# Kernel optimization log

Hardware: AMD Instinct MI355X
Metric: run time of the kernel (lower is better)

Reference implementation:

```python
import jax, jax.numpy as jnp
import numpy as np

N_SRC = 100000
N_DST = 100000
N_EDGES = 300000
FEAT = 256
REV_DIM = 128
REV_VOCAB = 500000


def setup_inputs() -> dict:
    key = jax.random.key(0)
    ks = jax.random.split(key, 14)
    feat = jax.random.normal(ks[0], (N_SRC, FEAT), dtype=jnp.float32)
    cj = jax.random.uniform(ks[1], (N_SRC, 1), dtype=jnp.float32)
    ci = jax.random.uniform(ks[2], (N_DST, 1), dtype=jnp.float32)
    edge_src = jax.random.randint(ks[3], (N_EDGES,), 0, N_SRC)
    edge_dst = jax.random.randint(ks[4], (N_EDGES,), 0, N_DST)
    review_id = jax.random.randint(ks[5], (N_EDGES,), 0, REV_VOCAB)
    s = 0.05
    review_emb = jax.random.normal(ks[6], (REV_VOCAB, REV_DIM), dtype=jnp.float32) * s
    prob_w = jax.random.normal(ks[7], (1, REV_DIM), dtype=jnp.float32) * s      # prob_score
    score_w = jax.random.normal(ks[8], (1, REV_DIM), dtype=jnp.float32) * s     # review_score
    rw1 = jax.random.normal(ks[9], (FEAT, REV_DIM), dtype=jnp.float32) * s      # review_w[0]
    rw2 = jax.random.normal(ks[10], (FEAT, FEAT), dtype=jnp.float32) * s        # review_w[2]
    rw3 = jax.random.normal(ks[11], (FEAT, FEAT), dtype=jnp.float32) * s        # review_w[4]
    lin_w = jax.random.normal(ks[12], (FEAT, FEAT), dtype=jnp.float32) * s      # self.linear
    lin_b = jax.random.normal(ks[13], (FEAT,), dtype=jnp.float32) * s
    return dict(feat=feat, cj=cj, ci=ci, edge_src=edge_src, edge_dst=edge_dst,
                review_id=review_id, review_emb=review_emb, prob_w=prob_w,
                score_w=score_w, rw1=rw1, rw2=rw2, rw3=rw3, lin_w=lin_w, lin_b=lin_b)


def reference(feat, cj, ci, edge_src, edge_dst, review_id,
              review_emb, prob_w, score_w, rw1, rw2, rw3, lin_w, lin_b):
    gelu = lambda x: jax.nn.gelu(x, approximate=False)  # torch default GELU (erf)
    # gather review embeddings per edge: [E, 128]
    rfeat = review_emb[review_id]
    pa = jax.nn.sigmoid(rfeat @ prob_w.T)    # [E, 1]
    ra = jax.nn.sigmoid(rfeat @ score_w.T)   # [E, 1]
    # review_w MLP: 128 -> F -> F -> F, no bias, GELU between
    rf = gelu(gelu(rfeat @ rw1.T) @ rw2.T) @ rw3.T  # [E, F]
    # per-edge message, gated and normalized by src cj (dropout is identity at p=0)
    m = (feat[edge_src] * pa + rf * ra) * cj[edge_src]  # [E, F]
    # scatter-sum to destination nodes
    h = jax.ops.segment_sum(m, edge_dst, num_segments=N_DST)  # [N_dst, F]
    rst = h * ci
    return rst @ lin_w.T + lin_b
```

## Files before the change

kernel.cpp:

```cpp
#include <hip/hip_runtime.h>
#include <math.h>
#include <stdint.h>


typedef short bf16x8 __attribute__((ext_vector_type(8)));
typedef float f32x16 __attribute__((ext_vector_type(16)));

__device__ __forceinline__ float bf2f(unsigned short v) {
    union { unsigned int u; float f; } x; x.u = ((unsigned int)v) << 16; return x.f;
}
__device__ __forceinline__ unsigned short f2bf(float f) {
    union { float f; unsigned int u; } x; x.f = f;
    unsigned int u = x.u;
    return (unsigned short)((u + 0x7FFFu + ((u >> 16) & 1u)) >> 16);
}
__device__ __forceinline__ unsigned pack2(float lo, float hi) {
    unsigned r;
    asm("v_cvt_pk_bf16_f32 %0, %1, %2" : "=v"(r) : "v"(lo), "v"(hi));
    return r;
}
__device__ __forceinline__ float gelu_fast(float x) {
    float y = x * (0.7978845608f + 0.0356774081f * x * x);
    float e = __builtin_amdgcn_exp2f(y * 2.8853900818f);
    float th = 1.0f - 2.0f * __builtin_amdgcn_rcpf(e + 1.0f);
    return 0.5f * x * (1.0f + th);
}
__device__ __forceinline__ float sigmoidf(float x) {
    return 1.0f / (1.0f + expf(-x));
}

__global__ __launch_bounds__(256) void prep_weights(
    const float* __restrict__ rw1, const float* __restrict__ rw2,
    const float* __restrict__ rw3, const float* __restrict__ lw,
    unsigned short* __restrict__ w1s, unsigned short* __restrict__ w2s,
    unsigned short* __restrict__ w3s, unsigned short* __restrict__ lws)
{
    int i = blockIdx.x * blockDim.x + threadIdx.x;
    int j   = i & 7;
    int l   = (i >> 3) & 31;
    int kgg = (i >> 8) & 1;
    int n2  = (i >> 9) & 7;
    int ks  = i >> 12;
    if (i < 32768) {
        w1s[i] = f2bf(rw1[(n2 * 32 + l) * 128 + ks * 16 + kgg * 8 + j]);
    }
    if (i < 65536) {
        int row = n2 * 32 + l, k = ks * 16 + kgg * 8 + j;
        w2s[i] = f2bf(rw2[(size_t)row * 256 + k]);
        w3s[i] = f2bf(rw3[(size_t)row * 256 + k]);
        int ok = (k & 192) | ((k & 1) << 5) | ((k & 63) >> 1);
        lws[i] = f2bf(lw[(size_t)row * 256 + ok]);
    }
}

__device__ __forceinline__ bf16x8 ldw(const unsigned short* __restrict__ W,
                                      int ks, int nglob, int kg, int l31) {
    return *(const bf16x8*)(W + (((((ks * 8 + nglob) * 2) + kg) * 32 + l31) << 3));
}

__global__ __launch_bounds__(256) void hist_kernel(
    const int* __restrict__ edst, int* __restrict__ cnt,
    int* __restrict__ within, int E)
{
    int e = blockIdx.x * blockDim.x + threadIdx.x;
    if (e < E) within[e] = atomicAdd(&cnt[edst[e]], 1);
}

__global__ __launch_bounds__(1024) void scan_block(
    const int* __restrict__ cnt, int* __restrict__ start,
    int* __restrict__ bsum, int n)
{
    __shared__ int s[1024];
    int gid = blockIdx.x * 1024 + threadIdx.x;
    int v = (gid < n) ? cnt[gid] : 0;
    s[threadIdx.x] = v;
    __syncthreads();
    #pragma unroll
    for (int off = 1; off < 1024; off <<= 1) {
        int t = (threadIdx.x >= off) ? s[threadIdx.x - off] : 0;
        __syncthreads();
        if (threadIdx.x >= off) s[threadIdx.x] += t;
        __syncthreads();
    }
    if (gid < n) start[gid] = s[threadIdx.x] - v;
    if (threadIdx.x == 1023) bsum[blockIdx.x] = s[1023];
}

__global__ void scan_bsum(int* __restrict__ bsum, int nb) {
    if (threadIdx.x == 0 && blockIdx.x == 0) {
        int acc = 0;
        for (int i = 0; i < nb; ++i) { int v = bsum[i]; bsum[i] = acc; acc += v; }
    }
}

__global__ __launch_bounds__(1024) void add_offsets(
    int* __restrict__ start, const int* __restrict__ bsum, int n, int E)
{
    int gid = blockIdx.x * 1024 + threadIdx.x;
    if (gid < n) start[gid] += bsum[gid >> 10];
    if (gid == 0) start[n] = E;
}

__global__ __launch_bounds__(256) void build_sorted(
    const int* __restrict__ edst, const int* __restrict__ within,
    const int* __restrict__ start, const int* __restrict__ rid,
    const int* __restrict__ esrc, int* __restrict__ rid_s,
    int* __restrict__ esrc_s, int E)
{
    int e = blockIdx.x * blockDim.x + threadIdx.x;
    if (e < E) {
        int pos = start[edst[e]] + within[e];
        rid_s[pos]  = rid[e];
        esrc_s[pos] = esrc[e];
    }
}

__device__ __forceinline__ bf16x8 ldtf(const unsigned short* t_lds, int row, int ks, int kg) {
    int slot = (ks * 2 + kg) ^ (row & 15);
    return *(const bf16x8*)((const char*)t_lds + row * 512 + slot * 16);
}
__device__ __forceinline__ void sttf(unsigned short* t_lds, int row, int nn, int p, int kg, uint2 w) {
    int slot = (nn * 4 + p) ^ (row & 15);
    *(uint2*)((char*)t_lds + row * 512 + slot * 16 + kg * 8) = w;
}
__device__ __forceinline__ bf16x8 ldrb(const unsigned short* t_rb, int row, int ks, int kg) {
    int slot = (ks * 2 + kg) ^ (row & 15);
    return *(const bf16x8*)((const char*)t_rb + row * 256 + slot * 16);
}

__global__ __launch_bounds__(256, 3) void fused_edge(
    const float* __restrict__ remb, const int* __restrict__ rid_s,
    const int* __restrict__ esrc_s,
    const unsigned short* __restrict__ w1s, const unsigned short* __restrict__ w2s,
    const unsigned short* __restrict__ w3s,
    const float* __restrict__ pw, const float* __restrict__ sw,
    const float* __restrict__ cj, float* __restrict__ ga,
    unsigned short* __restrict__ m, int E)
{
    __shared__ __align__(16) unsigned short t_lds[64 * 256];
    __shared__ __align__(16) unsigned short t_rb[64 * 128];
    __shared__ float gvb_lds[64];

    const int lane = threadIdx.x & 63;
    const int f    = threadIdx.x >> 6;
    const int l31  = lane & 31;
    const int kg   = lane >> 5;
    const int blk0 = blockIdx.x * 64;

    {
        const int t = threadIdx.x;
        #pragma unroll
        for (int p = 0; p < 4; ++p) {
            int sIdx = p * 256 + t;
            int row  = sIdx >> 4;
            int c16  = sIdx & 15;
            int gr   = blk0 + row;
            int rr   = rid_s[(gr < E) ? gr : (E - 1)];
            const float* sp = remb + (size_t)rr * 128 + c16 * 8;
            float4 a = *(const float4*)sp;
            float4 b = *(const float4*)(sp + 4);
            uint4 w;
            w.x = pack2(a.x, a.y); w.y = pack2(a.z, a.w);
            w.z = pack2(b.x, b.y); w.w = pack2(b.z, b.w);
            int slot = c16 ^ (row & 15);
            *(uint4*)((char*)t_rb + row * 256 + slot * 16) = w;
        }
    }
    __syncthreads();

    {
        f32x16 acc[2][2];
        #pragma unroll
        for (int g = 0; g < 2; ++g) { acc[g][0] = (f32x16)0.0f; acc[g][1] = (f32x16)0.0f; }
        float pd0 = 0.f, rd0 = 0.f, pd1 = 0.f, rd1 = 0.f;

        #pragma unroll
        for (int ks = 0; ks < 8; ++ks) {
            bf16x8 wf0 = ldw(w1s, ks, f * 2 + 0, kg, l31);
            bf16x8 wf1 = ldw(w1s, ks, f * 2 + 1, kg, l31);
            #pragma unroll
            for (int g = 0; g < 2; ++g) {
                bf16x8 af = ldrb(t_rb, g * 32 + l31, ks, kg);
                if (f == 0) {
                    const int kk = ks * 16 + kg * 8;
                    float4 p0 = *(const float4*)(pw + kk), p1 = *(const float4*)(pw + kk + 4);
                    float4 s0 = *(const float4*)(sw + kk), s1v = *(const float4*)(sw + kk + 4);
                    float v0 = bf2f((unsigned short)af[0]), v1 = bf2f((unsigned short)af[1]);
                    float v2 = bf2f((unsigned short)af[2]), v3 = bf2f((unsigned short)af[3]);
                    float v4 = bf2f((unsigned short)af[4]), v5 = bf2f((unsigned short)af[5]);
                    float v6 = bf2f((unsigned short)af[6]), v7 = bf2f((unsigned short)af[7]);
                    float dp = v0*p0.x + v1*p0.y + v2*p0.z + v3*p0.w
                             + v4*p1.x + v5*p1.y + v6*p1.z + v7*p1.w;
                    float dr = v0*s0.x + v1*s0.y + v2*s0.z + v3*s0.w
                             + v4*s1v.x + v5*s1v.y + v6*s1v.z + v7*s1v.w;
                    if (g == 0) { pd0 += dp; rd0 += dr; } else { pd1 += dp; rd1 += dr; }
                }
                acc[g][0] = __builtin_amdgcn_mfma_f32_32x32x16_bf16(wf0, af, acc[g][0], 0, 0, 0);
                acc[g][1] = __builtin_amdgcn_mfma_f32_32x32x16_bf16(wf1, af, acc[g][1], 0, 0, 0);
            }
        }

        if (f == 0) {
            pd0 += __shfl_xor(pd0, 32); rd0 += __shfl_xor(rd0, 32);
            pd1 += __shfl_xor(pd1, 32); rd1 += __shfl_xor(rd1, 32);
            if (lane < 32) {
                int i0 = blk0 + l31, i1 = blk0 + 32 + l31;
                float cj0 = cj[esrc_s[(i0 < E) ? i0 : (E - 1)]];
                float cj1 = cj[esrc_s[(i1 < E) ? i1 : (E - 1)]];
                if (i0 < E) ga[i0] = sigmoidf(pd0) * cj0;
                if (i1 < E) ga[i1] = sigmoidf(pd1) * cj1;
                gvb_lds[l31]      = sigmoidf(rd0) * cj0;
                gvb_lds[32 + l31] = sigmoidf(rd1) * cj1;
            }
        }

        #pragma unroll
        for (int g = 0; g < 2; ++g)
            #pragma unroll
            for (int n = 0; n < 2; ++n)
                #pragma unroll
                for (int p = 0; p < 4; ++p) {
                    uint2 w;
                    w.x = pack2(gelu_fast(acc[g][n][4*p + 0]), gelu_fast(acc[g][n][4*p + 1]));
                    w.y = pack2(gelu_fast(acc[g][n][4*p + 2]), gelu_fast(acc[g][n][4*p + 3]));
                    sttf(t_lds, g * 32 + l31, f * 2 + n, p, kg, w);
                }
    }
    __syncthreads();

    {
        f32x16 acc[2][2];
        #pragma unroll
        for (int g = 0; g < 2; ++g) { acc[g][0] = (f32x16)0.0f; acc[g][1] = (f32x16)0.0f; }

        #pragma unroll
        for (int ks = 0; ks < 16; ++ks) {
            bf16x8 wf0 = ldw(w2s, ks, f * 2 + 0, kg, l31);
            bf16x8 wf1 = ldw(w2s, ks, f * 2 + 1, kg, l31);
            #pragma unroll
            for (int g = 0; g < 2; ++g) {
                bf16x8 tf = ldtf(t_lds, g * 32 + l31, ks, kg);
                acc[g][0] = __builtin_amdgcn_mfma_f32_32x32x16_bf16(wf0, tf, acc[g][0], 0, 0, 0);
                acc[g][1] = __builtin_amdgcn_mfma_f32_32x32x16_bf16(wf1, tf, acc[g][1], 0, 0, 0);
            }
        }
        __syncthreads();
        #pragma unroll
        for (int g = 0; g < 2; ++g)
            #pragma unroll
            for (int n = 0; n < 2; ++n)
                #pragma unroll
                for (int p = 0; p < 4; ++p) {
                    uint2 w;
                    w.x = pack2(gelu_fast(acc[g][n][4*p + 0]), gelu_fast(acc[g][n][4*p + 1]));
                    w.y = pack2(gelu_fast(acc[g][n][4*p + 2]), gelu_fast(acc[g][n][4*p + 3]));
                    sttf(t_lds, g * 32 + l31, f * 2 + n, p, kg, w);
                }
    }
    __syncthreads();

    {
        f32x16 acc[2][2];
        #pragma unroll
        for (int g = 0; g < 2; ++g) { acc[g][0] = (f32x16)0.0f; acc[g][1] = (f32x16)0.0f; }

        #pragma unroll
        for (int ks = 0; ks < 16; ++ks) {
            bf16x8 wf0 = ldw(w3s, ks, f * 2 + 0, kg, l31);
            bf16x8 wf1 = ldw(w3s, ks, f * 2 + 1, kg, l31);
            #pragma unroll
            for (int g = 0; g < 2; ++g) {
                bf16x8 tf = ldtf(t_lds, g * 32 + l31, ks, kg);
                acc[g][0] = __builtin_amdgcn_mfma_f32_32x32x16_bf16(tf, wf0, acc[g][0], 0, 0, 0);
                acc[g][1] = __builtin_amdgcn_mfma_f32_32x32x16_bf16(tf, wf1, acc[g][1], 0, 0, 0);
            }
        }

        #pragma unroll
        for (int g = 0; g < 2; ++g)
            #pragma unroll
            for (int r = 0; r < 16; ++r) {
                const int lrow = (r & 3) + 8 * (r >> 2) + 4 * kg;
                const int gi = blk0 + g * 32 + lrow;
                if (gi < E) {
                    float gbv = gvb_lds[g * 32 + lrow];
                    float v0 = acc[g][0][r] * gbv;
                    float v1 = acc[g][1][r] * gbv;
                    *(unsigned*)(m + (size_t)gi * 256 + f * 64 + l31 * 2) = pack2(v0, v1);
                }
            }
    }
}

__global__ __launch_bounds__(256) void segsum_kernel(
    const int* __restrict__ start, const unsigned short* __restrict__ m,
    const float* __restrict__ ga, const int* __restrict__ esrc_s,
    const float* __restrict__ feat, unsigned short* __restrict__ h, int ND)
{
    int d = blockIdx.x * 4 + (threadIdx.x >> 6);
    if (d >= ND) return;
    int lane = threadIdx.x & 63;
    int q = lane >> 4;
    int b = lane & 15;
    int foff = q * 64 + 2 * b;
    int s0 = start[d], s1 = start[d + 1];
    float a0 = 0.f, a1 = 0.f, a2 = 0.f, a3 = 0.f;
    for (int base = s0; base < s1; base += 4) {
        float gav[4], msk[4];
        const float* fp[4];
        const unsigned short* mp[4];
        #pragma unroll
        for (int j = 0; j < 4; ++j) {
            int idx = base + j;
            bool v  = idx < s1;
            int ic  = v ? idx : (s1 - 1);
            msk[j]  = v ? 1.f : 0.f;
            gav[j]  = ga[ic] * msk[j];
            fp[j]   = feat + (size_t)esrc_s[ic] * 256 + foff;
            mp[j]   = m + (size_t)ic * 256 + lane * 4;
        }
        #pragma unroll
        for (int j = 0; j < 4; ++j) {
            float2 fa = *(const float2*)fp[j];
            float2 fb = *(const float2*)(fp[j] + 32);
            ushort4 v4 = *(const ushort4*)mp[j];
            a0 += bf2f(v4.x) * msk[j] + fa.x * gav[j];
            a1 += bf2f(v4.y) * msk[j] + fb.x * gav[j];
            a2 += bf2f(v4.z) * msk[j] + fa.y * gav[j];
            a3 += bf2f(v4.w) * msk[j] + fb.y * gav[j];
        }
    }
    ushort4 o; o.x = f2bf(a0); o.y = f2bf(a1); o.z = f2bf(a2); o.w = f2bf(a3);
    *(ushort4*)(h + (size_t)d * 256 + lane * 4) = o;
}

__global__ __launch_bounds__(256, 2) void g4_kernel(
    const unsigned short* __restrict__ Ab, const unsigned short* __restrict__ lws,
    float* __restrict__ outf, const float* __restrict__ ci,
    const float* __restrict__ bias, int M)
{
    const int lane = threadIdx.x & 63;
    const int wid  = threadIdx.x >> 6;
    const int l31  = lane & 31;
    const int kg   = lane >> 5;
    const int f    = wid & 1;
    const int wbase = blockIdx.x * 128 + (wid >> 1) * 64;
    const int r0 = wbase + l31, r1 = wbase + 32 + l31;
    const int ar0 = (r0 < M) ? r0 : (M - 1);
    const int ar1 = (r1 < M) ? r1 : (M - 1);

    f32x16 acc[2][4];
    #pragma unroll
    for (int mi = 0; mi < 2; ++mi)
        #pragma unroll
        for (int n = 0; n < 4; ++n) acc[mi][n] = (f32x16)0.0f;

    #pragma unroll
    for (int ks = 0; ks < 16; ++ks) {
        const int kk = ks * 16 + kg * 8;
        bf16x8 a0 = *(const bf16x8*)(Ab + (size_t)ar0 * 256 + kk);
        bf16x8 a1 = *(const bf16x8*)(Ab + (size_t)ar1 * 256 + kk);
        #pragma unroll
        for (int n = 0; n < 4; ++n) {
            bf16x8 b = ldw(lws, ks, f * 4 + n, kg, l31);
            acc[0][n] = __builtin_amdgcn_mfma_f32_32x32x16_bf16(a0, b, acc[0][n], 0, 0, 0);
            acc[1][n] = __builtin_amdgcn_mfma_f32_32x32x16_bf16(a1, b, acc[1][n], 0, 0, 0);
        }
    }
    #pragma unroll
    for (int mi = 0; mi < 2; ++mi) {
        #pragma unroll
        for (int r = 0; r < 16; ++r) {
            const int gr = wbase + mi * 32 + (r & 3) + 8 * (r >> 2) + 4 * kg;
            if (gr >= M) continue;
            float civ = ci[gr];
            #pragma unroll
            for (int n = 0; n < 4; ++n) {
                int col = f * 128 + n * 32 + l31;
                outf[(size_t)gr * 256 + col] = acc[mi][n][r] * civ + bias[col];
            }
        }
    }
}

extern "C" void kernel_launch(void* const* d_in, const int* in_sizes, int n_in,
                              void* d_out, int out_size, void* d_ws, size_t ws_size,
                              hipStream_t stream) {
    const float* feat = (const float*)d_in[0];
    const float* cj   = (const float*)d_in[1];
    const float* ci   = (const float*)d_in[2];
    const int*   esrc = (const int*)d_in[3];
    const int*   edst = (const int*)d_in[4];
    const int*   rid  = (const int*)d_in[5];
    const float* remb = (const float*)d_in[6];
    const float* pw   = (const float*)d_in[7];
    const float* sw   = (const float*)d_in[8];
    const float* rw1  = (const float*)d_in[9];
    const float* rw2  = (const float*)d_in[10];
    const float* rw3  = (const float*)d_in[11];
    const float* lw   = (const float*)d_in[12];
    const float* lb   = (const float*)d_in[13];
    float* out = (float*)d_out;

    const int E  = in_sizes[3];
    const int ND = in_sizes[2];

    char* ws = (char*)d_ws;
    float* ga = (float*)ws;
    unsigned short* m   = (unsigned short*)(ga + E);
    unsigned short* h   = m + (size_t)E * 256;
    unsigned short* w1s = h + (size_t)ND * 256;
    unsigned short* w2s = w1s + 32768;
    unsigned short* w3s = w2s + 65536;
    unsigned short* lws = w3s + 65536;
    int* cnt    = (int*)(lws + 65536);
    int* start  = cnt + ND;
    int* bsum   = start + ND + 1;
    int* within = bsum + 128;
    int* rid_s  = within + E;
    int* esrc_s = rid_s + E;

    const int NB = (ND + 1023) / 1024;

    hipMemsetAsync(cnt, 0, (size_t)ND * sizeof(int), stream);
    prep_weights<<<256, 256, 0, stream>>>(rw1, rw2, rw3, lw, w1s, w2s, w3s, lws);

    hist_kernel<<<(E + 255) / 256, 256, 0, stream>>>(edst, cnt, within, E);
    scan_block<<<NB, 1024, 0, stream>>>(cnt, start, bsum, ND);
    scan_bsum<<<1, 64, 0, stream>>>(bsum, NB);
    add_offsets<<<NB, 1024, 0, stream>>>(start, bsum, ND, E);
    build_sorted<<<(E + 255) / 256, 256, 0, stream>>>(edst, within, start, rid, esrc,
                                                      rid_s, esrc_s, E);

    fused_edge<<<(E + 63) / 64, 256, 0, stream>>>(
        remb, rid_s, esrc_s, w1s, w2s, w3s, pw, sw, cj, ga, m, E);

    segsum_kernel<<<(ND + 3) / 4, 256, 0, stream>>>(start, m, ga, esrc_s, feat, h, ND);

    g4_kernel<<<(ND + 127) / 128, 256, 0, stream>>>(h, lws, out, ci, lb, ND);
}
```

Measured before the change: 362.3 us.

## Store edge messages in natural column order and simplify GELU to sigmoid form

The MLP epilogue now uses lane shuffles so each even lane writes two adjacent columns, which puts the message buffer in natural column order. The segment-sum kernel can then read feat with one contiguous float4 per lane instead of two strided float2 loads, and the linear weight prep no longer needs its column permutation. GELU is replaced by the cheaper x*sigmoid(1.702x) approximation, which cuts instructions but is less accurate than the tanh form. The store pattern changes to half the lanes writing 4-byte words, which may hurt store coalescing.

```diff
diff --git a/kernel.cpp b/kernel.cpp
--- a/kernel.cpp
+++ b/kernel.cpp
@@ -20,10 +20,8 @@
     return r;
 }
 __device__ __forceinline__ float gelu_fast(float x) {
-    float y = x * (0.7978845608f + 0.0356774081f * x * x);
-    float e = __builtin_amdgcn_exp2f(y * 2.8853900818f);
-    float th = 1.0f - 2.0f * __builtin_amdgcn_rcpf(e + 1.0f);
-    return 0.5f * x * (1.0f + th);
+    float e = __builtin_amdgcn_exp2f(x * -2.4554912f);
+    return x * __builtin_amdgcn_rcpf(e + 1.0f);
 }
 __device__ __forceinline__ float sigmoidf(float x) {
     return 1.0f / (1.0f + expf(-x));
@@ -48,8 +46,7 @@
         int row = n2 * 32 + l, k = ks * 16 + kgg * 8 + j;
         w2s[i] = f2bf(rw2[(size_t)row * 256 + k]);
         w3s[i] = f2bf(rw3[(size_t)row * 256 + k]);
-        int ok = (k & 192) | ((k & 1) << 5) | ((k & 63) >> 1);
-        lws[i] = f2bf(lw[(size_t)row * 256 + ok]);
+        lws[i] = f2bf(lw[(size_t)row * 256 + k]);
     }
 }
 
@@ -282,11 +279,15 @@
             for (int r = 0; r < 16; ++r) {
                 const int lrow = (r & 3) + 8 * (r >> 2) + 4 * kg;
                 const int gi = blk0 + g * 32 + lrow;
-                if (gi < E) {
-                    float gbv = gvb_lds[g * 32 + lrow];
-                    float v0 = acc[g][0][r] * gbv;
-                    float v1 = acc[g][1][r] * gbv;
-                    *(unsigned*)(m + (size_t)gi * 256 + f * 64 + l31 * 2) = pack2(v0, v1);
+                float gbv = gvb_lds[g * 32 + lrow];
+                float v0 = acc[g][0][r] * gbv;
+                float v1 = acc[g][1][r] * gbv;
+                float o0 = __shfl_xor(v0, 1);
+                float o1 = __shfl_xor(v1, 1);
+                if (gi < E && (l31 & 1) == 0) {
+                    unsigned short* mp = m + (size_t)gi * 256 + f * 64 + l31;
+                    *(unsigned*)mp        = pack2(v0, o0);
+                    *(unsigned*)(mp + 32) = pack2(v1, o1);
                 }
             }
     }
@@ -300,9 +301,7 @@
     int d = blockIdx.x * 4 + (threadIdx.x >> 6);
     if (d >= ND) return;
     int lane = threadIdx.x & 63;
-    int q = lane >> 4;
-    int b = lane & 15;
-    int foff = q * 64 + 2 * b;
+    int coff = lane * 4;
     int s0 = start[d], s1 = start[d + 1];
     float a0 = 0.f, a1 = 0.f, a2 = 0.f, a3 = 0.f;
     for (int base = s0; base < s1; base += 4) {
@@ -316,22 +315,21 @@
             int ic  = v ? idx : (s1 - 1);
             msk[j]  = v ? 1.f : 0.f;
             gav[j]  = ga[ic] * msk[j];
-            fp[j]   = feat + (size_t)esrc_s[ic] * 256 + foff;
-            mp[j]   = m + (size_t)ic * 256 + lane * 4;
+            fp[j]   = feat + (size_t)esrc_s[ic] * 256 + coff;
+            mp[j]   = m + (size_t)ic * 256 + coff;
         }
         #pragma unroll
         for (int j = 0; j < 4; ++j) {
-            float2 fa = *(const float2*)fp[j];
-            float2 fb = *(const float2*)(fp[j] + 32);
+            float4 fv = *(const float4*)fp[j];
             ushort4 v4 = *(const ushort4*)mp[j];
-            a0 += bf2f(v4.x) * msk[j] + fa.x * gav[j];
-            a1 += bf2f(v4.y) * msk[j] + fb.x * gav[j];
-            a2 += bf2f(v4.z) * msk[j] + fa.y * gav[j];
-            a3 += bf2f(v4.w) * msk[j] + fb.y * gav[j];
+            a0 += bf2f(v4.x) * msk[j] + fv.x * gav[j];
+            a1 += bf2f(v4.y) * msk[j] + fv.y * gav[j];
+            a2 += bf2f(v4.z) * msk[j] + fv.z * gav[j];
+            a3 += bf2f(v4.w) * msk[j] + fv.w * gav[j];
         }
     }
     ushort4 o; o.x = f2bf(a0); o.y = f2bf(a1); o.z = f2bf(a2); o.w = f2bf(a3);
-    *(ushort4*)(h + (size_t)d * 256 + lane * 4) = o;
+    *(ushort4*)(h + (size_t)d * 256 + coff) = o;
 }
 
 __global__ __launch_bounds__(256, 2) void g4_kernel(
```

Result: no change. 358.9 us (-1.0%).
